# Optimization experiments

Measured on AMD Instinct MI355X. Metric: run time of the kernel, lower is better.

The kernel has to match this reference:

```python
import jax, jax.numpy as jnp
import numpy as np

B, H, S, D = 2, 16, 4096, 64

def setup_inputs() -> dict:
    key = jax.random.key(0)
    kq, kk, kv = jax.random.split(key, 3)
    Q = jax.random.normal(kq, (B, H, S, D), dtype=jnp.float32)
    K = jax.random.normal(kk, (B, H, S, D), dtype=jnp.float32)
    V = jax.random.normal(kv, (B, H, S, D), dtype=jnp.float32)
    return {"Q": Q, "K": K, "V": V}

def reference(Q, K, V):
    # scores: [B, H, S, S] = Q @ K^T, scaled by 1/sqrt(D) BEFORE softmax
    scale = 1.0 / jnp.sqrt(jnp.asarray(Q.shape[-1], Q.dtype))
    scores = jnp.einsum('bhqd,bhkd->bhqk', Q, K) * scale
    attn = jax.nn.softmax(scores, axis=-1)
    # output: [B, H, S, D]
    return jnp.einsum('bhqk,bhkd->bhqd', attn, V)
```

## Files before the change

kernel.cpp:

```cpp
#include <hip/hip_runtime.h>
#include <hip/hip_bf16.h>

namespace {

constexpr int kS  = 4096;
constexpr int kD  = 64;
constexpr int kQB = 256;
constexpr int kKVT = 128;
constexpr int kBH = 2 * 16;
constexpr int kNT = kS / kKVT;
constexpr int kNWG = (kS / kQB) * kBH;
constexpr int kTileE = kKVT * kD;

typedef __attribute__((ext_vector_type(8))) short bf16x8;
typedef __attribute__((ext_vector_type(4))) short s16x4;
typedef __attribute__((ext_vector_type(4))) float f32x4;
typedef unsigned short u16;

constexpr float SCL  = 0.18033688011112042f;
constexpr float BIAS = -8.0f;

__device__ __forceinline__ u16 f2bf(float f) {
  union { __hip_bfloat16 h; u16 u; } c;
  c.h = __float2bfloat16(f);
  return c.u;
}

__device__ __forceinline__ void gload_lds16(const void* g, void* l) {
  __builtin_amdgcn_global_load_lds(
      (const __attribute__((address_space(1))) unsigned int*)g,
      (__attribute__((address_space(3))) unsigned int*)l, 16, 0, 0);
}

__device__ __forceinline__ int vt_idx64(int d, int k) {
  const int swz = (((d >> 4) & 3) << 4) ^ ((d & 15) << 2);
  return d * 64 + (k ^ swz);
}

__global__ __launch_bounds__(256)
void cvt_k_vt(const float* __restrict__ K, const float* __restrict__ V,
              u16* __restrict__ Kb, u16* __restrict__ Vtg, int n16, int nKBlk) {
  __shared__ __align__(16) u16 Vts[kTileE];
  const int t = threadIdx.x;
  if ((int)blockIdx.x < nKBlk) {
    const int i = blockIdx.x * 256 + t;
    if (i >= n16) return;
#pragma unroll
    for (int h = 0; h < 2; ++h) {
      const size_t e = (size_t)i * 16 + h * 8;
      const float4 a = *(const float4*)(K + e);
      const float4 b = *(const float4*)(K + e + 4);
      union { u16 us[8]; uint4 q; } p;
      p.us[0] = f2bf(a.x); p.us[1] = f2bf(a.y);
      p.us[2] = f2bf(a.z); p.us[3] = f2bf(a.w);
      p.us[4] = f2bf(b.x); p.us[5] = f2bf(b.y);
      p.us[6] = f2bf(b.z); p.us[7] = f2bf(b.w);
      *(uint4*)(Kb + e) = p.q;
    }
    return;
  }
  const int v    = blockIdx.x - nKBlk;
  const int head = v >> 5;
  const int tile = v & 31;
  const float* Vt0 = V + (size_t)head * kS * kD + (size_t)tile * kKVT * kD;
  const int k0 = (t & 31) * 4;
  const int d0 = (t >> 5) * 8;
  const int half = k0 >> 6;
  const int kl   = k0 & 63;
  float4 ra[4], rb[4];
#pragma unroll
  for (int i = 0; i < 4; ++i) {
    ra[i] = *(const float4*)(Vt0 + (k0 + i) * kD + d0);
    rb[i] = *(const float4*)(Vt0 + (k0 + i) * kD + d0 + 4);
  }
#pragma unroll
  for (int j = 0; j < 8; ++j) {
    float c0, c1, c2, c3;
    if (j < 4) {
      c0 = (&ra[0].x)[j];     c1 = (&ra[1].x)[j];
      c2 = (&ra[2].x)[j];     c3 = (&ra[3].x)[j];
    } else {
      c0 = (&rb[0].x)[j - 4]; c1 = (&rb[1].x)[j - 4];
      c2 = (&rb[2].x)[j - 4]; c3 = (&rb[3].x)[j - 4];
    }
    s16x4 col;
    col[0] = (short)f2bf(c0); col[1] = (short)f2bf(c1);
    col[2] = (short)f2bf(c2); col[3] = (short)f2bf(c3);
    *(s16x4*)&Vts[half * 4096 + vt_idx64(d0 + j, kl)] = col;
  }
  __syncthreads();
  u16* dst = Vtg + (size_t)(head * 32 + tile) * kTileE;
#pragma unroll
  for (int p = 0; p < 4; ++p)
    *(uint4*)(dst + p * 2048 + t * 8) = *(const uint4*)&Vts[p * 2048 + t * 8];
}

__global__ __launch_bounds__(512)
void attn_fwd_bf16(const float* __restrict__ Qg, const u16* __restrict__ Kb,
                   const u16* __restrict__ Vtg, float* __restrict__ Og) {
  __shared__ __align__(16) u16 Klds[2][kTileE];
  __shared__ __align__(16) u16 Vt[2][kTileE];

  const int tid  = threadIdx.x;
  const int lane = tid & 63;
  const int w    = tid >> 6;
  const int g    = lane >> 4;
  const int lq   = lane & 15;

  const int wg   = (blockIdx.x & 7) * (kNWG / 8) + (blockIdx.x >> 3);
  const int bh   = wg >> 4;
  const int qblk = wg & 15;

  const size_t base = (size_t)bh * kS * kD;
  const int qb = qblk * kQB + w * 32;

  bf16x8 qf[2][2];
#pragma unroll
  for (int st = 0; st < 2; ++st) {
    const float* qp = Qg + base + (size_t)(qb + st * 16 + lq) * kD + 8 * g;
#pragma unroll
    for (int dh = 0; dh < 2; ++dh) {
      const float4 a = *(const float4*)(qp + dh * 32);
      const float4 b = *(const float4*)(qp + dh * 32 + 4);
      bf16x8 f;
      f[0] = (short)f2bf(a.x * SCL); f[1] = (short)f2bf(a.y * SCL);
      f[2] = (short)f2bf(a.z * SCL); f[3] = (short)f2bf(a.w * SCL);
      f[4] = (short)f2bf(b.x * SCL); f[5] = (short)f2bf(b.y * SCL);
      f[6] = (short)f2bf(b.z * SCL); f[7] = (short)f2bf(b.w * SCL);
      qf[st][dh] = f;
    }
  }

  bf16x8 onesf;
#pragma unroll
  for (int i = 0; i < 8; ++i) onesf[i] = (short)0x3F80;

  f32x4 oacc[2][4];
#pragma unroll
  for (int st = 0; st < 2; ++st)
#pragma unroll
    for (int dt = 0; dt < 4; ++dt) oacc[st][dt] = f32x4{0.f, 0.f, 0.f, 0.f};
  f32x4 lacc[2] = {{0.f, 0.f, 0.f, 0.f}, {0.f, 0.f, 0.f, 0.f}};

  const u16* Kh  = Kb + base;
  const u16* Vth = Vtg + base;

  auto stageK = [&](const u16* Ktile, u16* Kbuf) {
    const int wv = w - 4;
#pragma unroll
    for (int p = 0; p < 4; ++p) {
      const int L = wv * 4096 + p * 1024 + lane * 16;
      const int row = L >> 7;
      const int colb = (L & 127) ^ ((row & 7) << 4);
      gload_lds16(Ktile + row * kD + (colb >> 1), Kbuf + (wv * 2048 + p * 512));
    }
  };
  auto stageV = [&](const u16* Vtile, u16* Vbuf) {
#pragma unroll
    for (int p = 0; p < 4; ++p)
      gload_lds16(Vtile + w * 2048 + p * 512 + lane * 8,
                  Vbuf + (w * 2048 + p * 512));
  };

  if (w >= 4) stageK(Kh, Klds[0]);
  else        stageV(Vth, Vt[0]);
  __syncthreads();

  const f32x4 cbias = {BIAS, BIAS, BIAS, BIAS};

  int cur = 0;
  for (int t = 0; t < kNT; ++t) {
    const bool pf = (t + 1 < kNT);
    if (pf) {
      if (w >= 4) stageK(Kh + (size_t)(t + 1) * kTileE, Klds[cur ^ 1]);
      else        stageV(Vth + (size_t)(t + 1) * kTileE, Vt[cur ^ 1]);
    }

#pragma unroll
    for (int sub = 0; sub < 2; ++sub) {
      f32x4 s[2][4];
      __builtin_amdgcn_s_setprio(1);
#pragma unroll
      for (int kt = 0; kt < 4; ++kt) {
        const int krow = sub * 64 + kt * 16 + lq;
        const char* kbp = (const char*)Klds[cur] + krow * 128;
        const int sw = (krow & 7) << 4;
        const bf16x8 kf0 = *(const bf16x8*)(kbp + ((16 * g) ^ sw));
        const bf16x8 kf1 = *(const bf16x8*)(kbp + ((16 * g + 64) ^ sw));
#pragma unroll
        for (int st = 0; st < 2; ++st) {
          f32x4 acc = __builtin_amdgcn_mfma_f32_16x16x32_bf16(
              kf0, qf[st][0], cbias, 0, 0, 0);
          s[st][kt] = __builtin_amdgcn_mfma_f32_16x16x32_bf16(
              kf1, qf[st][1], acc, 0, 0, 0);
        }
      }
      __builtin_amdgcn_s_setprio(0);

      bf16x8 pfr[2][2];
#pragma unroll
      for (int st = 0; st < 2; ++st) {
#pragma unroll
        for (int kt = 0; kt < 4; ++kt)
#pragma unroll
          for (int rr = 0; rr < 4; ++rr)
            s[st][kt][rr] = __builtin_amdgcn_exp2f(s[st][kt][rr]);
#pragma unroll
        for (int kc = 0; kc < 2; ++kc) {
          bf16x8 f;
#pragma unroll
          for (int i = 0; i < 4; ++i) {
            f[i]     = (short)f2bf(s[st][2 * kc][i]);
            f[4 + i] = (short)f2bf(s[st][2 * kc + 1][i]);
          }
          pfr[st][kc] = f;
        }
      }

      __builtin_amdgcn_s_setprio(1);
#pragma unroll
      for (int st = 0; st < 2; ++st)
#pragma unroll
        for (int kc = 0; kc < 2; ++kc)
          lacc[st] = __builtin_amdgcn_mfma_f32_16x16x32_bf16(
              onesf, pfr[st][kc], lacc[st], 0, 0, 0);
      const u16* Vsub = &Vt[cur][sub * 4096];
#pragma unroll
      for (int dt = 0; dt < 4; ++dt) {
        const int d = dt * 16 + lq;
#pragma unroll
        for (int kc = 0; kc < 2; ++kc) {
          const s16x4 lo = *(const s16x4*)&Vsub[vt_idx64(d, kc * 32 + 4 * g)];
          const s16x4 hi = *(const s16x4*)&Vsub[vt_idx64(d, kc * 32 + 16 + 4 * g)];
          const bf16x8 vf =
              __builtin_shufflevector(lo, hi, 0, 1, 2, 3, 4, 5, 6, 7);
#pragma unroll
          for (int st = 0; st < 2; ++st)
            oacc[st][dt] = __builtin_amdgcn_mfma_f32_16x16x32_bf16(
                vf, pfr[st][kc], oacc[st][dt], 0, 0, 0);
        }
      }
      __builtin_amdgcn_s_setprio(0);
    }

    __syncthreads();
    cur ^= 1;
  }

#pragma unroll
  for (int st = 0; st < 2; ++st) {
    const float inv = 1.0f / lacc[st][0];
    float* op = Og + base + (size_t)(qb + st * 16 + lq) * kD;
#pragma unroll
    for (int dt = 0; dt < 4; ++dt) {
      f32x4 o = oacc[st][dt];
      o *= inv;
      *(f32x4*)(op + dt * 16 + 4 * g) = o;
    }
  }
}

__global__ __launch_bounds__(256)
void attn_fwd_f32(const float* __restrict__ Qg, const float* __restrict__ Kg,
                  const float* __restrict__ Vg, float* __restrict__ Og) {
  __shared__ __align__(16) u16 Klds[64 * kD];
  __shared__ __align__(16) u16 Vts[kD * 64];

  const int tid  = threadIdx.x;
  const int lane = tid & 63;
  const int w    = tid >> 6;
  const int g    = lane >> 4;
  const int lq   = lane & 15;

  const size_t base = (size_t)blockIdx.y * kS * kD;
  const int qb = blockIdx.x * 128 + w * 32;

  bf16x8 qf[2][2];
#pragma unroll
  for (int st = 0; st < 2; ++st) {
    const float* qp = Qg + base + (size_t)(qb + st * 16 + lq) * kD + 8 * g;
#pragma unroll
    for (int dh = 0; dh < 2; ++dh) {
      const float4 a = *(const float4*)(qp + dh * 32);
      const float4 b = *(const float4*)(qp + dh * 32 + 4);
      bf16x8 f;
      f[0] = (short)f2bf(a.x * SCL); f[1] = (short)f2bf(a.y * SCL);
      f[2] = (short)f2bf(a.z * SCL); f[3] = (short)f2bf(a.w * SCL);
      f[4] = (short)f2bf(b.x * SCL); f[5] = (short)f2bf(b.y * SCL);
      f[6] = (short)f2bf(b.z * SCL); f[7] = (short)f2bf(b.w * SCL);
      qf[st][dh] = f;
    }
  }

  f32x4 oacc[2][4];
#pragma unroll
  for (int st = 0; st < 2; ++st)
#pragma unroll
    for (int dt = 0; dt < 4; ++dt) oacc[st][dt] = f32x4{0.f, 0.f, 0.f, 0.f};
  float m_run[2] = {-__builtin_inff(), -__builtin_inff()};
  float l_run[2] = {0.0f, 0.0f};

  const int r  = tid >> 2;
  const int c0 = (tid & 3) * 16;

  for (int kv = 0; kv < kS; kv += 64) {
    __syncthreads();
    {
      const float* kp = Kg + base + (size_t)(kv + r) * kD + c0;
      const float* vp = Vg + base + (size_t)(kv + r) * kD + c0;
      float4 kq[4], vq[4];
#pragma unroll
      for (int j = 0; j < 4; ++j) kq[j] = *(const float4*)(kp + 4 * j);
#pragma unroll
      for (int j = 0; j < 4; ++j) vq[j] = *(const float4*)(vp + 4 * j);
      const float* kfp = (const float*)kq;
      const float* vfp = (const float*)vq;
      union { u16 us[8]; uint4 q; } p0, p1;
#pragma unroll
      for (int j = 0; j < 8; ++j) {
        p0.us[j] = f2bf(kfp[j]);
        p1.us[j] = f2bf(kfp[8 + j]);
      }
      char* kb = (char*)Klds + r * 128;
      const int sw = (r & 7) << 4;
      *(uint4*)(kb + ((c0 * 2) ^ sw))      = p0.q;
      *(uint4*)(kb + ((c0 * 2 + 16) ^ sw)) = p1.q;
#pragma unroll
      for (int j = 0; j < 16; ++j) Vts[vt_idx64(c0 + j, r)] = f2bf(vfp[j]);
    }
    __syncthreads();

    f32x4 s[2][4];
#pragma unroll
    for (int kt = 0; kt < 4; ++kt) {
      const int krow = kt * 16 + lq;
      const char* kb = (const char*)Klds + krow * 128;
      const int sw = (krow & 7) << 4;
      const bf16x8 kf0 = *(const bf16x8*)(kb + ((16 * g) ^ sw));
      const bf16x8 kf1 = *(const bf16x8*)(kb + ((16 * g + 64) ^ sw));
#pragma unroll
      for (int st = 0; st < 2; ++st) {
        f32x4 acc = __builtin_amdgcn_mfma_f32_16x16x32_bf16(
            kf0, qf[st][0], f32x4{0.f, 0.f, 0.f, 0.f}, 0, 0, 0);
        s[st][kt] = __builtin_amdgcn_mfma_f32_16x16x32_bf16(
            kf1, qf[st][1], acc, 0, 0, 0);
      }
    }

    bf16x8 pfr[2][2];
#pragma unroll
    for (int st = 0; st < 2; ++st) {
      float mx = s[st][0][0];
#pragma unroll
      for (int kt = 0; kt < 4; ++kt)
#pragma unroll
        for (int rr = 0; rr < 4; ++rr) mx = fmaxf(mx, s[st][kt][rr]);
      mx = fmaxf(mx, __shfl_xor(mx, 16));
      mx = fmaxf(mx, __shfl_xor(mx, 32));
      const float mnew  = fmaxf(m_run[st], mx);
      const float alpha = exp2f(m_run[st] - mnew);
      m_run[st] = mnew;
      float ps = 0.0f;
#pragma unroll
      for (int kt = 0; kt < 4; ++kt)
#pragma unroll
        for (int rr = 0; rr < 4; ++rr) {
          const float e = exp2f(s[st][kt][rr] - mnew);
          s[st][kt][rr] = e;
          ps += e;
        }
      ps += __shfl_xor(ps, 16);
      ps += __shfl_xor(ps, 32);
      l_run[st] = l_run[st] * alpha + ps;
#pragma unroll
      for (int dt = 0; dt < 4; ++dt) oacc[st][dt] *= alpha;
#pragma unroll
      for (int kc = 0; kc < 2; ++kc) {
        bf16x8 f;
#pragma unroll
        for (int i = 0; i < 4; ++i) {
          f[i]     = (short)f2bf(s[st][2 * kc][i]);
          f[4 + i] = (short)f2bf(s[st][2 * kc + 1][i]);
        }
        pfr[st][kc] = f;
      }
    }

#pragma unroll
    for (int dt = 0; dt < 4; ++dt) {
      const int d = dt * 16 + lq;
#pragma unroll
      for (int kc = 0; kc < 2; ++kc) {
        const s16x4 lo = *(const s16x4*)&Vts[vt_idx64(d, kc * 32 + 4 * g)];
        const s16x4 hi = *(const s16x4*)&Vts[vt_idx64(d, kc * 32 + 16 + 4 * g)];
        const bf16x8 vf =
            __builtin_shufflevector(lo, hi, 0, 1, 2, 3, 4, 5, 6, 7);
#pragma unroll
        for (int st = 0; st < 2; ++st)
          oacc[st][dt] = __builtin_amdgcn_mfma_f32_16x16x32_bf16(
              vf, pfr[st][kc], oacc[st][dt], 0, 0, 0);
      }
    }
  }

#pragma unroll
  for (int st = 0; st < 2; ++st) {
    const float inv = 1.0f / l_run[st];
    float* op = Og + base + (size_t)(qb + st * 16 + lq) * kD;
#pragma unroll
    for (int dt = 0; dt < 4; ++dt) {
      f32x4 o = oacc[st][dt];
      o *= inv;
      *(f32x4*)(op + dt * 16 + 4 * g) = o;
    }
  }
}

}

extern "C" void kernel_launch(void* const* d_in, const int* in_sizes, int n_in,
                              void* d_out, int out_size, void* d_ws, size_t ws_size,
                              hipStream_t stream) {
  const float* Q = (const float*)d_in[0];
  const float* K = (const float*)d_in[1];
  const float* V = (const float*)d_in[2];
  float* O = (float*)d_out;
  const int n = in_sizes[0];
  const size_t tbytes = (size_t)n * 2;

  if (ws_size >= 2 * tbytes) {
    u16* Kb  = (u16*)d_ws;
    u16* Vtg = Kb + n;
    const int n16  = n / 16;
    const int nKBlk = (n16 + 255) / 256;
    const int nVBlk = kBH * (kS / kKVT);
    cvt_k_vt<<<nKBlk + nVBlk, 256, 0, stream>>>(K, V, Kb, Vtg, n16, nKBlk);
    attn_fwd_bf16<<<dim3(kNWG), 512, 0, stream>>>(Q, Kb, Vtg, O);
  } else {
    dim3 grid(kS / 128, kBH);
    attn_fwd_f32<<<grid, 256, 0, stream>>>(Q, K, V, O);
  }
}
```

Before: 153.0 us.

## Switch attention MFMAs to 32x32x16 with pre-permuted K/V tile images

Replaces the 16x16x32 bf16 MFMA tiles with 32x32x16 MFMAs, so each wave handles 32 query rows as a single block. The preprocessing kernel now writes K and V into fragment-ordered tile images, with V permuted to match the P register layout. The attention kernel can then load operands with contiguous 16-byte LDS reads and plain linear global-to-LDS copies, with no swizzle math. The intent is fewer MFMA issues and less LDS address work per tile. The costs are larger accumulator register footprints and a new layout that has to match the MFMA fragment mapping exactly.

```diff
diff --git a/kernel.cpp b/kernel.cpp
--- a/kernel.cpp
+++ b/kernel.cpp
@@ -13,12 +13,16 @@
 constexpr int kTileE = kKVT * kD;
 
 typedef __attribute__((ext_vector_type(8))) short bf16x8;
-typedef __attribute__((ext_vector_type(4))) short s16x4;
 typedef __attribute__((ext_vector_type(4))) float f32x4;
+typedef __attribute__((ext_vector_type(16))) float f32x16;
 typedef unsigned short u16;
 
 constexpr float SCL  = 0.18033688011112042f;
 constexpr float BIAS = -8.0f;
+
+__device__ __forceinline__ int pvperm(int s) {
+  return (s & 3) + 8 * ((s >> 2) & 1) + 4 * (s >> 3);
+}
 
 __device__ __forceinline__ u16 f2bf(float f) {
   union { __hip_bfloat16 h; u16 u; } c;
@@ -32,74 +36,221 @@
       (__attribute__((address_space(3))) unsigned int*)l, 16, 0, 0);
 }
 
+__global__ __launch_bounds__(256)
+void build_imgs(const float* __restrict__ K, const float* __restrict__ V,
+                u16* __restrict__ Kimg, u16* __restrict__ Vimg, int nKTile) {
+  __shared__ float Vf[kKVT][kD];
+  const int t = threadIdx.x;
+  if ((int)blockIdx.x < nKTile) {
+    const int v    = blockIdx.x;
+    const int head = v >> 5;
+    const int tile = v & 31;
+    const float* Kt0 = K + (size_t)head * kS * kD + (size_t)tile * kKVT * kD;
+    u16* dst = Kimg + (size_t)v * kTileE;
+    const int row  = t >> 1;
+    const int half = t & 1;
+    const float* src = Kt0 + row * kD + half * 32;
+    float4 a[8];
+#pragma unroll
+    for (int i = 0; i < 8; ++i) a[i] = *(const float4*)(src + 4 * i);
+    const float* fp = (const float*)a;
+    const int grp = row >> 5;
+#pragma unroll
+    for (int kh = 0; kh < 2; ++kh) {
+      const int kq = 2 * half + kh;
+      union { u16 us[16]; uint4 q[2]; } p;
+#pragma unroll
+      for (int s = 0; s < 16; ++s) p.us[s] = f2bf(fp[16 * kh + s]);
+      u16* bp = dst + (grp * 4 + kq) * 512 + (row & 31) * 16;
+      *(uint4*)(bp)     = p.q[0];
+      *(uint4*)(bp + 8) = p.q[1];
+    }
+    return;
+  }
+  const int v    = blockIdx.x - nKTile;
+  const int head = v >> 5;
+  const int tile = v & 31;
+  const float* Vt0 = V + (size_t)head * kS * kD + (size_t)tile * kKVT * kD;
+#pragma unroll
+  for (int i = 0; i < 8; ++i) {
+    const int f4 = t * 8 + i;
+    const int row = f4 >> 4, c4 = f4 & 15;
+    *(float4*)&Vf[row][c4 * 4] = *(const float4*)(Vt0 + row * kD + c4 * 4);
+  }
+  __syncthreads();
+  u16* dst = Vimg + (size_t)v * kTileE;
+  const int b  = t >> 5;
+  const int l5 = t & 31;
+  const int kvb = 64 * (b >> 2) + 32 * ((b >> 1) & 1) + 16 * (b & 1);
+#pragma unroll
+  for (int dd = 0; dd < 2; ++dd) {
+    const int d = 2 * l5 + dd;
+    union { u16 us[16]; uint4 q[2]; } p;
+#pragma unroll
+    for (int s = 0; s < 16; ++s) p.us[s] = f2bf(Vf[kvb + pvperm(s)][d]);
+    u16* bp = dst + b * 1024 + d * 16;
+    *(uint4*)(bp)     = p.q[0];
+    *(uint4*)(bp + 8) = p.q[1];
+  }
+}
+
+__global__ __launch_bounds__(512)
+void attn_fwd_bf16(const float* __restrict__ Qg, const u16* __restrict__ Kimg,
+                   const u16* __restrict__ Vimg, float* __restrict__ Og) {
+  __shared__ __align__(16) u16 Klds[2][kTileE];
+  __shared__ __align__(16) u16 Vlds[2][kTileE];
+
+  const int tid  = threadIdx.x;
+  const int lane = tid & 63;
+  const int w    = tid >> 6;
+  const int l31  = lane & 31;
+  const int h    = lane >> 5;
+
+  const int wg   = (blockIdx.x & 7) * (kNWG / 8) + (blockIdx.x >> 3);
+  const int bh   = wg >> 4;
+  const int qblk = wg & 15;
+
+  const size_t base = (size_t)bh * kS * kD;
+  const int qb = qblk * kQB + w * 32;
+
+  bf16x8 qf[4];
+  {
+    const float* qp = Qg + base + (size_t)(qb + l31) * kD;
+#pragma unroll
+    for (int kq = 0; kq < 4; ++kq) {
+      const float4 a = *(const float4*)(qp + 16 * kq + 8 * h);
+      const float4 b = *(const float4*)(qp + 16 * kq + 8 * h + 4);
+      bf16x8 f;
+      f[0] = (short)f2bf(a.x * SCL); f[1] = (short)f2bf(a.y * SCL);
+      f[2] = (short)f2bf(a.z * SCL); f[3] = (short)f2bf(a.w * SCL);
+      f[4] = (short)f2bf(b.x * SCL); f[5] = (short)f2bf(b.y * SCL);
+      f[6] = (short)f2bf(b.z * SCL); f[7] = (short)f2bf(b.w * SCL);
+      qf[kq] = f;
+    }
+  }
+
+  bf16x8 onesf;
+#pragma unroll
+  for (int i = 0; i < 8; ++i) onesf[i] = (short)0x3F80;
+
+  f32x16 oacc[2];
+  oacc[0] = (f32x16)(0.f);
+  oacc[1] = (f32x16)(0.f);
+  f32x16 lacc = (f32x16)(0.f);
+  f32x16 cbias = (f32x16)(BIAS);
+
+  const u16* Kh = Kimg + base;
+  const u16* Vh = Vimg + base;
+
+  auto stage = [&](const u16* src, u16* dstl) {
+    const int wv = w & 3;
+#pragma unroll
+    for (int p = 0; p < 4; ++p)
+      gload_lds16(src + wv * 2048 + p * 512 + lane * 8,
+                  dstl + wv * 2048 + p * 512 + lane * 8);
+  };
+
+  if (w >= 4) stage(Kh, Klds[0]);
+  else        stage(Vh, Vlds[0]);
+  __syncthreads();
+
+  int cur = 0;
+  for (int t = 0; t < kNT; ++t) {
+    const bool pf = (t + 1 < kNT);
+    if (pf) {
+      if (w >= 4) stage(Kh + (size_t)(t + 1) * kTileE, Klds[cur ^ 1]);
+      else        stage(Vh + (size_t)(t + 1) * kTileE, Vlds[cur ^ 1]);
+    }
+
+#pragma unroll
+    for (int sub = 0; sub < 2; ++sub) {
+      f32x16 s[2];
+      __builtin_amdgcn_s_setprio(1);
+#pragma unroll
+      for (int T = 0; T < 2; ++T) {
+        f32x16 acc = cbias;
+#pragma unroll
+        for (int kq = 0; kq < 4; ++kq) {
+          const bf16x8 kf = *(const bf16x8*)
+              &Klds[cur][(sub * 8 + T * 4 + kq) * 512 + l31 * 16 + h * 8];
+          acc = __builtin_amdgcn_mfma_f32_32x32x16_bf16(kf, qf[kq], acc,
+                                                        0, 0, 0);
+        }
+        s[T] = acc;
+      }
+      __builtin_amdgcn_s_setprio(0);
+
+#pragma unroll
+      for (int T = 0; T < 2; ++T)
+#pragma unroll
+        for (int r = 0; r < 16; ++r)
+          s[T][r] = __builtin_amdgcn_exp2f(s[T][r]);
+
+      bf16x8 pfr[2][2];
+#pragma unroll
+      for (int T = 0; T < 2; ++T)
+#pragma unroll
+        for (int n = 0; n < 2; ++n) {
+          bf16x8 f;
+#pragma unroll
+          for (int j = 0; j < 8; ++j)
+            f[j] = (short)f2bf(s[T][8 * n + j]);
+          pfr[T][n] = f;
+        }
+
+      __builtin_amdgcn_s_setprio(1);
+#pragma unroll
+      for (int T = 0; T < 2; ++T)
+#pragma unroll
+        for (int n = 0; n < 2; ++n)
+          lacc = __builtin_amdgcn_mfma_f32_32x32x16_bf16(onesf, pfr[T][n],
+                                                         lacc, 0, 0, 0);
+#pragma unroll
+      for (int dt = 0; dt < 2; ++dt)
+#pragma unroll
+        for (int T = 0; T < 2; ++T)
+#pragma unroll
+          for (int n = 0; n < 2; ++n) {
+            const bf16x8 vf = *(const bf16x8*)
+                &Vlds[cur][(sub * 4 + T * 2 + n) * 1024 + dt * 512 +
+                           l31 * 16 + h * 8];
+            oacc[dt] = __builtin_amdgcn_mfma_f32_32x32x16_bf16(
+                vf, pfr[T][n], oacc[dt], 0, 0, 0);
+          }
+      __builtin_amdgcn_s_setprio(0);
+    }
+
+    __syncthreads();
+    cur ^= 1;
+  }
+
+  {
+    const float inv = 1.0f / lacc[0];
+    float* op = Og + base + (size_t)(qb + l31) * kD;
+#pragma unroll
+    for (int dt = 0; dt < 2; ++dt)
+#pragma unroll
+      for (int m = 0; m < 4; ++m) {
+        f32x4 o = {oacc[dt][4 * m + 0], oacc[dt][4 * m + 1],
+                   oacc[dt][4 * m + 2], oacc[dt][4 * m + 3]};
+        o *= inv;
+        *(f32x4*)(op + 32 * dt + 8 * m + 4 * h) = o;
+      }
+  }
+}
+
 __device__ __forceinline__ int vt_idx64(int d, int k) {
   const int swz = (((d >> 4) & 3) << 4) ^ ((d & 15) << 2);
   return d * 64 + (k ^ swz);
 }
 
+typedef __attribute__((ext_vector_type(4))) short s16x4;
+
 __global__ __launch_bounds__(256)
-void cvt_k_vt(const float* __restrict__ K, const float* __restrict__ V,
-              u16* __restrict__ Kb, u16* __restrict__ Vtg, int n16, int nKBlk) {
-  __shared__ __align__(16) u16 Vts[kTileE];
-  const int t = threadIdx.x;
-  if ((int)blockIdx.x < nKBlk) {
-    const int i = blockIdx.x * 256 + t;
-    if (i >= n16) return;
-#pragma unroll
-    for (int h = 0; h < 2; ++h) {
-      const size_t e = (size_t)i * 16 + h * 8;
-      const float4 a = *(const float4*)(K + e);
-      const float4 b = *(const float4*)(K + e + 4);
-      union { u16 us[8]; uint4 q; } p;
-      p.us[0] = f2bf(a.x); p.us[1] = f2bf(a.y);
-      p.us[2] = f2bf(a.z); p.us[3] = f2bf(a.w);
-      p.us[4] = f2bf(b.x); p.us[5] = f2bf(b.y);
-      p.us[6] = f2bf(b.z); p.us[7] = f2bf(b.w);
-      *(uint4*)(Kb + e) = p.q;
-    }
-    return;
-  }
-  const int v    = blockIdx.x - nKBlk;
-  const int head = v >> 5;
-  const int tile = v & 31;
-  const float* Vt0 = V + (size_t)head * kS * kD + (size_t)tile * kKVT * kD;
-  const int k0 = (t & 31) * 4;
-  const int d0 = (t >> 5) * 8;
-  const int half = k0 >> 6;
-  const int kl   = k0 & 63;
-  float4 ra[4], rb[4];
-#pragma unroll
-  for (int i = 0; i < 4; ++i) {
-    ra[i] = *(const float4*)(Vt0 + (k0 + i) * kD + d0);
-    rb[i] = *(const float4*)(Vt0 + (k0 + i) * kD + d0 + 4);
-  }
-#pragma unroll
-  for (int j = 0; j < 8; ++j) {
-    float c0, c1, c2, c3;
-    if (j < 4) {
-      c0 = (&ra[0].x)[j];     c1 = (&ra[1].x)[j];
-      c2 = (&ra[2].x)[j];     c3 = (&ra[3].x)[j];
-    } else {
-      c0 = (&rb[0].x)[j - 4]; c1 = (&rb[1].x)[j - 4];
-      c2 = (&rb[2].x)[j - 4]; c3 = (&rb[3].x)[j - 4];
-    }
-    s16x4 col;
-    col[0] = (short)f2bf(c0); col[1] = (short)f2bf(c1);
-    col[2] = (short)f2bf(c2); col[3] = (short)f2bf(c3);
-    *(s16x4*)&Vts[half * 4096 + vt_idx64(d0 + j, kl)] = col;
-  }
-  __syncthreads();
-  u16* dst = Vtg + (size_t)(head * 32 + tile) * kTileE;
-#pragma unroll
-  for (int p = 0; p < 4; ++p)
-    *(uint4*)(dst + p * 2048 + t * 8) = *(const uint4*)&Vts[p * 2048 + t * 8];
-}
-
-__global__ __launch_bounds__(512)
-void attn_fwd_bf16(const float* __restrict__ Qg, const u16* __restrict__ Kb,
-                   const u16* __restrict__ Vtg, float* __restrict__ Og) {
-  __shared__ __align__(16) u16 Klds[2][kTileE];
-  __shared__ __align__(16) u16 Vt[2][kTileE];
+void attn_fwd_f32(const float* __restrict__ Qg, const float* __restrict__ Kg,
+                  const float* __restrict__ Vg, float* __restrict__ Og) {
+  __shared__ __align__(16) u16 Klds[64 * kD];
+  __shared__ __align__(16) u16 Vts[kD * 64];
 
   const int tid  = threadIdx.x;
   const int lane = tid & 63;
@@ -107,12 +258,8 @@
   const int g    = lane >> 4;
   const int lq   = lane & 15;
 
-  const int wg   = (blockIdx.x & 7) * (kNWG / 8) + (blockIdx.x >> 3);
-  const int bh   = wg >> 4;
-  const int qblk = wg & 15;
-
-  const size_t base = (size_t)bh * kS * kD;
-  const int qb = qblk * kQB + w * 32;
+  const size_t base = (size_t)blockIdx.y * kS * kD;
+  const int qb = blockIdx.x * 128 + w * 32;
 
   bf16x8 qf[2][2];
 #pragma unroll
@@ -131,167 +278,6 @@
     }
   }
 
-  bf16x8 onesf;
-#pragma unroll
-  for (int i = 0; i < 8; ++i) onesf[i] = (short)0x3F80;
-
-  f32x4 oacc[2][4];
-#pragma unroll
-  for (int st = 0; st < 2; ++st)
-#pragma unroll
-    for (int dt = 0; dt < 4; ++dt) oacc[st][dt] = f32x4{0.f, 0.f, 0.f, 0.f};
-  f32x4 lacc[2] = {{0.f, 0.f, 0.f, 0.f}, {0.f, 0.f, 0.f, 0.f}};
-
-  const u16* Kh  = Kb + base;
-  const u16* Vth = Vtg + base;
-
-  auto stageK = [&](const u16* Ktile, u16* Kbuf) {
-    const int wv = w - 4;
-#pragma unroll
-    for (int p = 0; p < 4; ++p) {
-      const int L = wv * 4096 + p * 1024 + lane * 16;
-      const int row = L >> 7;
-      const int colb = (L & 127) ^ ((row & 7) << 4);
-      gload_lds16(Ktile + row * kD + (colb >> 1), Kbuf + (wv * 2048 + p * 512));
-    }
-  };
-  auto stageV = [&](const u16* Vtile, u16* Vbuf) {
-#pragma unroll
-    for (int p = 0; p < 4; ++p)
-      gload_lds16(Vtile + w * 2048 + p * 512 + lane * 8,
-                  Vbuf + (w * 2048 + p * 512));
-  };
-
-  if (w >= 4) stageK(Kh, Klds[0]);
-  else        stageV(Vth, Vt[0]);
-  __syncthreads();
-
-  const f32x4 cbias = {BIAS, BIAS, BIAS, BIAS};
-
-  int cur = 0;
-  for (int t = 0; t < kNT; ++t) {
-    const bool pf = (t + 1 < kNT);
-    if (pf) {
-      if (w >= 4) stageK(Kh + (size_t)(t + 1) * kTileE, Klds[cur ^ 1]);
-      else        stageV(Vth + (size_t)(t + 1) * kTileE, Vt[cur ^ 1]);
-    }
-
-#pragma unroll
-    for (int sub = 0; sub < 2; ++sub) {
-      f32x4 s[2][4];
-      __builtin_amdgcn_s_setprio(1);
-#pragma unroll
-      for (int kt = 0; kt < 4; ++kt) {
-        const int krow = sub * 64 + kt * 16 + lq;
-        const char* kbp = (const char*)Klds[cur] + krow * 128;
-        const int sw = (krow & 7) << 4;
-        const bf16x8 kf0 = *(const bf16x8*)(kbp + ((16 * g) ^ sw));
-        const bf16x8 kf1 = *(const bf16x8*)(kbp + ((16 * g + 64) ^ sw));
-#pragma unroll
-        for (int st = 0; st < 2; ++st) {
-          f32x4 acc = __builtin_amdgcn_mfma_f32_16x16x32_bf16(
-              kf0, qf[st][0], cbias, 0, 0, 0);
-          s[st][kt] = __builtin_amdgcn_mfma_f32_16x16x32_bf16(
-              kf1, qf[st][1], acc, 0, 0, 0);
-        }
-      }
-      __builtin_amdgcn_s_setprio(0);
-
-      bf16x8 pfr[2][2];
-#pragma unroll
-      for (int st = 0; st < 2; ++st) {
-#pragma unroll
-        for (int kt = 0; kt < 4; ++kt)
-#pragma unroll
-          for (int rr = 0; rr < 4; ++rr)
-            s[st][kt][rr] = __builtin_amdgcn_exp2f(s[st][kt][rr]);
-#pragma unroll
-        for (int kc = 0; kc < 2; ++kc) {
-          bf16x8 f;
-#pragma unroll
-          for (int i = 0; i < 4; ++i) {
-            f[i]     = (short)f2bf(s[st][2 * kc][i]);
-            f[4 + i] = (short)f2bf(s[st][2 * kc + 1][i]);
-          }
-          pfr[st][kc] = f;
-        }
-      }
-
-      __builtin_amdgcn_s_setprio(1);
-#pragma unroll
-      for (int st = 0; st < 2; ++st)
-#pragma unroll
-        for (int kc = 0; kc < 2; ++kc)
-          lacc[st] = __builtin_amdgcn_mfma_f32_16x16x32_bf16(
-              onesf, pfr[st][kc], lacc[st], 0, 0, 0);
-      const u16* Vsub = &Vt[cur][sub * 4096];
-#pragma unroll
-      for (int dt = 0; dt < 4; ++dt) {
-        const int d = dt * 16 + lq;
-#pragma unroll
-        for (int kc = 0; kc < 2; ++kc) {
-          const s16x4 lo = *(const s16x4*)&Vsub[vt_idx64(d, kc * 32 + 4 * g)];
-          const s16x4 hi = *(const s16x4*)&Vsub[vt_idx64(d, kc * 32 + 16 + 4 * g)];
-          const bf16x8 vf =
-              __builtin_shufflevector(lo, hi, 0, 1, 2, 3, 4, 5, 6, 7);
-#pragma unroll
-          for (int st = 0; st < 2; ++st)
-            oacc[st][dt] = __builtin_amdgcn_mfma_f32_16x16x32_bf16(
-                vf, pfr[st][kc], oacc[st][dt], 0, 0, 0);
-        }
-      }
-      __builtin_amdgcn_s_setprio(0);
-    }
-
-    __syncthreads();
-    cur ^= 1;
-  }
-
-#pragma unroll
-  for (int st = 0; st < 2; ++st) {
-    const float inv = 1.0f / lacc[st][0];
-    float* op = Og + base + (size_t)(qb + st * 16 + lq) * kD;
-#pragma unroll
-    for (int dt = 0; dt < 4; ++dt) {
-      f32x4 o = oacc[st][dt];
-      o *= inv;
-      *(f32x4*)(op + dt * 16 + 4 * g) = o;
-    }
-  }
-}
-
-__global__ __launch_bounds__(256)
-void attn_fwd_f32(const float* __restrict__ Qg, const float* __restrict__ Kg,
-                  const float* __restrict__ Vg, float* __restrict__ Og) {
-  __shared__ __align__(16) u16 Klds[64 * kD];
-  __shared__ __align__(16) u16 Vts[kD * 64];
-
-  const int tid  = threadIdx.x;
-  const int lane = tid & 63;
-  const int w    = tid >> 6;
-  const int g    = lane >> 4;
-  const int lq   = lane & 15;
-
-  const size_t base = (size_t)blockIdx.y * kS * kD;
-  const int qb = blockIdx.x * 128 + w * 32;
-
-  bf16x8 qf[2][2];
-#pragma unroll
-  for (int st = 0; st < 2; ++st) {
-    const float* qp = Qg + base + (size_t)(qb + st * 16 + lq) * kD + 8 * g;
-#pragma unroll
-    for (int dh = 0; dh < 2; ++dh) {
-      const float4 a = *(const float4*)(qp + dh * 32);
-      const float4 b = *(const float4*)(qp + dh * 32 + 4);
-      bf16x8 f;
-      f[0] = (short)f2bf(a.x * SCL); f[1] = (short)f2bf(a.y * SCL);
-      f[2] = (short)f2bf(a.z * SCL); f[3] = (short)f2bf(a.w * SCL);
-      f[4] = (short)f2bf(b.x * SCL); f[5] = (short)f2bf(b.y * SCL);
-      f[6] = (short)f2bf(b.z * SCL); f[7] = (short)f2bf(b.w * SCL);
-      qf[st][dh] = f;
-    }
-  }
-
   f32x4 oacc[2][4];
 #pragma unroll
   for (int st = 0; st < 2; ++st)
@@ -429,13 +415,11 @@
   const size_t tbytes = (size_t)n * 2;
 
   if (ws_size >= 2 * tbytes) {
-    u16* Kb  = (u16*)d_ws;
-    u16* Vtg = Kb + n;
-    const int n16  = n / 16;
-    const int nKBlk = (n16 + 255) / 256;
-    const int nVBlk = kBH * (kS / kKVT);
-    cvt_k_vt<<<nKBlk + nVBlk, 256, 0, stream>>>(K, V, Kb, Vtg, n16, nKBlk);
-    attn_fwd_bf16<<<dim3(kNWG), 512, 0, stream>>>(Q, Kb, Vtg, O);
+    u16* Kimg = (u16*)d_ws;
+    u16* Vimg = Kimg + n;
+    const int nKTile = kBH * (kS / kKVT);
+    build_imgs<<<2 * nKTile, 256, 0, stream>>>(K, V, Kimg, Vimg, nKTile);
+    attn_fwd_bf16<<<dim3(kNWG), 512, 0, stream>>>(Q, Kimg, Vimg, O);
   } else {
     dim3 grid(kS / 128, kBH);
     attn_fwd_f32<<<grid, 256, 0, stream>>>(Q, K, V, O);
```

After: 162.9 us. +6.4%, slower.
